# Kernel optimization log

Measured on AMD Instinct MI355X. Metric: run time of the kernel, lower is better.

## Reference

```python
import jax, jax.numpy as jnp
import numpy as np

ROWS, COLS, DIM, BATCH = 128, 128, 64, 128

def setup_inputs() -> dict:
    key = jax.random.key(0)
    kx, kw = jax.random.split(key)
    x = jax.random.normal(kx, (BATCH, DIM), dtype=jnp.float32)
    # SOM codebook weights, randomly initialized as in _initialize_weights()
    weights = jax.random.normal(kw, (ROWS, COLS, DIM), dtype=jnp.float32)
    return {"x": x, "weights": weights}

def reference(x, weights):
    # Squared Euclidean distance from each input to every grid neuron.
    # x: (B, D); weights: (R, C, D) -> distances: (B, R, C)
    diff = weights[None, :, :, :] - x[:, None, None, :]
    distances = jnp.sum(diff * diff, axis=-1)
    return distances
```

## Files before the change

### kernel.cpp

```cpp
#include <hip/hip_runtime.h>


#define SOM_B   128
#define SOM_D   64
#define SOM_N   16384
#define SOM_BT  8
#define SOM_TPB 256

__global__ __launch_bounds__(SOM_TPB, 4)
void som_dist_kernel(const float* __restrict__ x,
                     const float* __restrict__ w,
                     float* __restrict__ out) {
    __shared__ float x2s[SOM_BT];

    const int tid = threadIdx.x;
    const int n   = blockIdx.x * SOM_TPB + tid;
    const int b0  = blockIdx.y * SOM_BT;

    if (tid < SOM_BT) {
        const float4* xr = (const float4*)(x + (size_t)(b0 + tid) * SOM_D);
        float s = 0.f;
        #pragma unroll
        for (int i = 0; i < 16; ++i) {
            float4 v = xr[i];
            s += v.x * v.x + v.y * v.y + v.z * v.z + v.w * v.w;
        }
        x2s[tid] = s;
    }

    float4 wr[16];
    {
        const float4* wg = (const float4*)(w + (size_t)n * SOM_D);
        #pragma unroll
        for (int i = 0; i < 16; ++i) wr[i] = wg[i];
    }
    float wn2 = 0.f;
    #pragma unroll
    for (int i = 0; i < 16; ++i) {
        wn2 += wr[i].x * wr[i].x + wr[i].y * wr[i].y
             + wr[i].z * wr[i].z + wr[i].w * wr[i].w;
    }

    __syncthreads();

    #pragma unroll
    for (int b = 0; b < SOM_BT; ++b) {
        const float* __restrict__ xb = x + (size_t)(b0 + b) * SOM_D;
        float acc = 0.f;
        #pragma unroll
        for (int i = 0; i < 16; ++i) {
            acc += wr[i].x * xb[4 * i + 0] + wr[i].y * xb[4 * i + 1]
                 + wr[i].z * xb[4 * i + 2] + wr[i].w * xb[4 * i + 3];
        }
        out[(size_t)(b0 + b) * SOM_N + n] =
            __builtin_fmaf(-2.f, acc, wn2 + x2s[b]);
    }
}

extern "C" void kernel_launch(void* const* d_in, const int* in_sizes, int n_in,
                              void* d_out, int out_size, void* d_ws, size_t ws_size,
                              hipStream_t stream) {
    const float* x = (const float*)d_in[0];
    const float* w = (const float*)d_in[1];
    float* out = (float*)d_out;

    dim3 grid(SOM_N / SOM_TPB, SOM_B / SOM_BT);
    dim3 block(SOM_TPB);
    som_dist_kernel<<<grid, block, 0, stream>>>(x, w, out);
}
```

Before: 72.51 us.

## Compute SOM distance cross term with bf16x3 split MFMA instead of scalar FMA

Replaces the per-thread scalar dot-product loop with MFMA 16x16x32 bf16 instructions. To keep near-fp32 accuracy, each fp32 operand is split into hi and lo bf16 parts and the product uses three MFMAs per K-chunk. Blocks are retiled to 64 neurons by 32 batch rows, and neuron norms are precomputed into shared memory. The kernel is dominated by writing the 8 MB output, so the compute savings may matter less than the store pattern. The new stores write 16 contiguous floats per row, which may coalesce worse than before, and the bf16 split adds rounding error.

```diff
diff --git a/kernel.cpp b/kernel.cpp
--- a/kernel.cpp
+++ b/kernel.cpp
@@ -4,21 +4,40 @@
 #define SOM_B   128
 #define SOM_D   64
 #define SOM_N   16384
-#define SOM_BT  8
 #define SOM_TPB 256
+#define BLK_N   64
+#define BLK_BQ  32
+
+typedef __bf16 bf16x8 __attribute__((ext_vector_type(8)));
+typedef float  f32x4  __attribute__((ext_vector_type(4)));
+
+__device__ __forceinline__ void split8(float4 f0, float4 f1,
+                                       bf16x8* hi, bf16x8* lo) {
+    float f[8] = {f0.x, f0.y, f0.z, f0.w, f1.x, f1.y, f1.z, f1.w};
+    bf16x8 h, l;
+    #pragma unroll
+    for (int j = 0; j < 8; ++j) {
+        __bf16 hj = (__bf16)f[j];
+        h[j] = hj;
+        l[j] = (__bf16)(f[j] - (float)hj);
+    }
+    *hi = h;
+    *lo = l;
+}
 
 __global__ __launch_bounds__(SOM_TPB, 4)
 void som_dist_kernel(const float* __restrict__ x,
                      const float* __restrict__ w,
                      float* __restrict__ out) {
-    __shared__ float x2s[SOM_BT];
+    __shared__ float x2s[BLK_BQ];
+    __shared__ float wn2s[BLK_N];
 
     const int tid = threadIdx.x;
-    const int n   = blockIdx.x * SOM_TPB + tid;
-    const int b0  = blockIdx.y * SOM_BT;
+    const int nb0 = blockIdx.x * BLK_N;
+    const int bq  = blockIdx.y * BLK_BQ;
 
-    if (tid < SOM_BT) {
-        const float4* xr = (const float4*)(x + (size_t)(b0 + tid) * SOM_D);
+    if (tid < BLK_BQ) {
+        const float4* xr = (const float4*)(x + (size_t)(bq + tid) * SOM_D);
         float s = 0.f;
         #pragma unroll
         for (int i = 0; i < 16; ++i) {
@@ -26,34 +45,64 @@
             s += v.x * v.x + v.y * v.y + v.z * v.z + v.w * v.w;
         }
         x2s[tid] = s;
+    } else if (tid < BLK_BQ + BLK_N) {
+        const int j = tid - BLK_BQ;
+        const float4* wr = (const float4*)(w + (size_t)(nb0 + j) * SOM_D);
+        float s = 0.f;
+        #pragma unroll
+        for (int i = 0; i < 16; ++i) {
+            float4 v = wr[i];
+            s += v.x * v.x + v.y * v.y + v.z * v.z + v.w * v.w;
+        }
+        wn2s[j] = s;
     }
-
-    float4 wr[16];
-    {
-        const float4* wg = (const float4*)(w + (size_t)n * SOM_D);
-        #pragma unroll
-        for (int i = 0; i < 16; ++i) wr[i] = wg[i];
-    }
-    float wn2 = 0.f;
-    #pragma unroll
-    for (int i = 0; i < 16; ++i) {
-        wn2 += wr[i].x * wr[i].x + wr[i].y * wr[i].y
-             + wr[i].z * wr[i].z + wr[i].w * wr[i].w;
-    }
-
     __syncthreads();
 
+    const int wv = tid >> 6;
+    const int l  = tid & 63;
+    const int lr = l & 15;
+    const int lg = l >> 4;
+    const int nc = nb0 + wv * 16;
+
+    const float* wrow = w + (size_t)(nc + lr) * SOM_D + lg * 8;
+    float4 wf0 = *(const float4*)(wrow + 0);
+    float4 wf1 = *(const float4*)(wrow + 4);
+    float4 wf2 = *(const float4*)(wrow + 32);
+    float4 wf3 = *(const float4*)(wrow + 36);
+    bf16x8 bh0, bl0, bh1, bl1;
+    split8(wf0, wf1, &bh0, &bl0);
+    split8(wf2, wf3, &bh1, &bl1);
+
+    const float wn2v = wn2s[wv * 16 + lr];
+
     #pragma unroll
-    for (int b = 0; b < SOM_BT; ++b) {
-        const float* __restrict__ xb = x + (size_t)(b0 + b) * SOM_D;
-        float acc = 0.f;
+    for (int sub = 0; sub < 2; ++sub) {
+        const int br = bq + sub * 16;
+        const float* xrow = x + (size_t)(br + lr) * SOM_D + lg * 8;
+        float4 xf0 = *(const float4*)(xrow + 0);
+        float4 xf1 = *(const float4*)(xrow + 4);
+        float4 xf2 = *(const float4*)(xrow + 32);
+        float4 xf3 = *(const float4*)(xrow + 36);
+        bf16x8 ah0, al0, ah1, al1;
+        split8(xf0, xf1, &ah0, &al0);
+        split8(xf2, xf3, &ah1, &al1);
+
+        f32x4 acc = {0.f, 0.f, 0.f, 0.f};
+        acc = __builtin_amdgcn_mfma_f32_16x16x32_bf16(ah0, bh0, acc, 0, 0, 0);
+        acc = __builtin_amdgcn_mfma_f32_16x16x32_bf16(al0, bh0, acc, 0, 0, 0);
+        acc = __builtin_amdgcn_mfma_f32_16x16x32_bf16(ah0, bl0, acc, 0, 0, 0);
+        acc = __builtin_amdgcn_mfma_f32_16x16x32_bf16(ah1, bh1, acc, 0, 0, 0);
+        acc = __builtin_amdgcn_mfma_f32_16x16x32_bf16(al1, bh1, acc, 0, 0, 0);
+        acc = __builtin_amdgcn_mfma_f32_16x16x32_bf16(ah1, bl1, acc, 0, 0, 0);
+
+        const float4 x2v = *(const float4*)&x2s[sub * 16 + lg * 4];
+        const float xx[4] = {x2v.x, x2v.y, x2v.z, x2v.w};
         #pragma unroll
-        for (int i = 0; i < 16; ++i) {
-            acc += wr[i].x * xb[4 * i + 0] + wr[i].y * xb[4 * i + 1]
-                 + wr[i].z * xb[4 * i + 2] + wr[i].w * xb[4 * i + 3];
+        for (int i = 0; i < 4; ++i) {
+            const int row = br + lg * 4 + i;
+            out[(size_t)row * SOM_N + nc + lr] =
+                __builtin_fmaf(-2.f, acc[i], wn2v + xx[i]);
         }
-        out[(size_t)(b0 + b) * SOM_N + n] =
-            __builtin_fmaf(-2.f, acc, wn2 + x2s[b]);
     }
 }
 
@@ -64,7 +113,7 @@
     const float* w = (const float*)d_in[1];
     float* out = (float*)d_out;
 
-    dim3 grid(SOM_N / SOM_TPB, SOM_B / SOM_BT);
+    dim3 grid(SOM_N / BLK_N, SOM_B / BLK_BQ);
     dim3 block(SOM_TPB);
     som_dist_kernel<<<grid, block, 0, stream>>>(x, w, out);
 }
```

After: 67.79 us. -6.5%, faster.
